# Kernel optimization log

Hardware: AMD Instinct MI355X
Metric: run time of the kernel (lower is better)

## Reference

```python
import jax, jax.numpy as jnp
import numpy as np

T, B, H, L = 64, 128, 256, 2  # steps/stack_size, batch, hidden, layers


def setup_inputs() -> dict:
    key = jax.random.key(0)
    ks = jax.random.split(key, 6)
    s = 1.0 / np.sqrt(H)
    x = jax.random.normal(ks[0], (T, B, H), dtype=jnp.float32)
    ops = jax.random.randint(ks[1], (T, B), 0, 2, dtype=jnp.int32)  # push=1, hold=0
    W_ih = jax.random.uniform(ks[2], (L, 4 * H, H), jnp.float32, -s, s)
    W_hh = jax.random.uniform(ks[3], (L, 4 * H, H), jnp.float32, -s, s)
    b_ih = jax.random.uniform(ks[4], (L, 4 * H), jnp.float32, -s, s)
    b_hh = jax.random.uniform(ks[5], (L, 4 * H), jnp.float32, -s, s)
    return {"x": x, "ops": ops, "W_ih": W_ih, "W_hh": W_hh, "b_ih": b_ih, "b_hh": b_hh}


def reference(x, ops, W_ih, W_hh, b_ih, b_hh):
    T_, B_, H_ = x.shape
    L_ = W_ih.shape[0]
    bidx = jnp.arange(B_)

    def cell(xt, h_prev, c_prev):
        # multi-layer LSTM cell; layer l>0 takes layer l-1 hidden as input (dropout=0)
        inp = xt
        hs, cs = [], []
        for l in range(L_):
            gates = inp @ W_ih[l].T + b_ih[l] + h_prev[..., l] @ W_hh[l].T + b_hh[l]
            i, f, g, o = jnp.split(gates, 4, axis=-1)
            c = jax.nn.sigmoid(f) * c_prev[..., l] + jax.nn.sigmoid(i) * jnp.tanh(g)
            h = jax.nn.sigmoid(o) * jnp.tanh(c)
            hs.append(h)
            cs.append(c)
            inp = h
        return jnp.stack(hs, axis=-1), jnp.stack(cs, axis=-1)  # (B, H, L)

    def step(carry, xt_op):
        hstack, cstack, pos = carry  # stacks: (T+1, B, H, L), pos: (B,)
        xt, opt = xt_op
        h_prev = hstack[pos, bidx]  # gather top-of-stack, (B, H, L)
        c_prev = cstack[pos, bidx]
        nh, nc = cell(xt, h_prev, c_prev)
        # hold_or_push writes at pos+1 for every batch element, then pos += op
        hstack = hstack.at[pos + 1, bidx].set(nh)
        cstack = cstack.at[pos + 1, bidx].set(nc)
        pos = pos + opt
        return (hstack, cstack, pos), nh[..., -1]  # last-layer hidden output

    hs0 = jnp.zeros((T_ + 1, B_, H_, L_), dtype=x.dtype)
    cs0 = jnp.zeros((T_ + 1, B_, H_, L_), dtype=x.dtype)
    pos0 = jnp.zeros((B_,), dtype=jnp.int32)
    _, outs = jax.lax.scan(step, (hs0, cs0, pos0), (x, ops))
    return outs  # (T, B, H)
```

## Files before the change

### kernel.cpp

```cpp
#include <hip/hip_runtime.h>
#include <hip/hip_fp16.h>
#include <cstddef>

#define TT 64
#define BB 128
#define HH 256
#define G4 1024
#define BLK 256
#define NBG 32
#define NHG 16

#define OFF_XG     0u
#define OFF_WTIH0  8388608u
#define OFF_HX0    8650752u
#define OFF_HX1    8716288u

__device__ __forceinline__ float sigf(float x) { return 1.0f / (1.0f + expf(-x)); }

typedef _Float16 h2v __attribute__((ext_vector_type(2)));

__device__ __forceinline__ float dot2acc(unsigned w, unsigned h, float acc) {
#if __has_builtin(__builtin_amdgcn_fdot2)
  return __builtin_amdgcn_fdot2(__builtin_bit_cast(h2v, w),
                                __builtin_bit_cast(h2v, h), acc, false);
#else
  __half2 wv = *(__half2*)&w, hv = *(__half2*)&h;
  float2 wf = __half22float2(wv), hf = __half22float2(hv);
  return fmaf(wf.x, hf.x, fmaf(wf.y, hf.y, acc));
#endif
}

__device__ __forceinline__ unsigned packh2(float e, float o) {
  return (unsigned)__half_as_ushort(__float2half(e)) |
         ((unsigned)__half_as_ushort(__float2half(o)) << 16);
}

__global__ void transpose1(const float* __restrict__ W_ih, float* __restrict__ ws) {
  __shared__ float tile[32][33];
  float* dst = ws + OFF_WTIH0;
  const int g0 = blockIdx.x * 32, k0 = blockIdx.y * 32;
  const int tx = threadIdx.x, ty = threadIdx.y;
#pragma unroll
  for (int i = 0; i < 32; i += 8)
    tile[ty + i][tx] = W_ih[(size_t)(g0 + ty + i) * HH + k0 + tx];
  __syncthreads();
#pragma unroll
  for (int i = 0; i < 32; i += 8)
    dst[(size_t)(k0 + ty + i) * G4 + g0 + tx] = tile[tx][ty + i];
}

__global__ void xg_kernel(const float* __restrict__ x,
                          const float* __restrict__ b_ih,
                          float* __restrict__ ws) {
  const float* __restrict__ WTih0 = ws + OFF_WTIH0;
  float* __restrict__ Xg = ws + OFF_XG;
  const int r0 = blockIdx.x * 16;
  const int g = blockIdx.y * 256 + threadIdx.x;
  __shared__ float xs[16][HH];
  for (int i = threadIdx.x; i < 16 * HH; i += 256)
    xs[i >> 8][i & 255] = x[(size_t)(r0 + (i >> 8)) * HH + (i & 255)];
  __syncthreads();
  float acc[16];
  const float bias = b_ih[g];
#pragma unroll
  for (int r = 0; r < 16; ++r) acc[r] = bias;
  for (int k = 0; k < HH; ++k) {
    const float w = WTih0[(size_t)k * G4 + g];
#pragma unroll
    for (int r = 0; r < 16; ++r) acc[r] = fmaf(xs[r][k], w, acc[r]);
  }
  const int hg = (g >> 4) & 15;
  const int lc = ((g >> 8) << 4) | (g & 15);
#pragma unroll
  for (int r = 0; r < 16; ++r) {
    const int rr = r0 + r;
    const int t = rr >> 7, b = rr & 127;
    Xg[(((size_t)t * NHG + hg) * 128 + b) * 64 + lc] = acc[r];
  }
}

__global__ void __launch_bounds__(BLK, 2)
seq7(const float* __restrict__ W_ih,
     const float* __restrict__ W_hh,
     const float* __restrict__ b_ih,
     const float* __restrict__ b_hh,
     const int* __restrict__ ops,
     float* __restrict__ ws,
     float* __restrict__ out) {
  const int bg = blockIdx.x & 31;
  const int hg = blockIdx.x >> 5;
  const int tid = threadIdx.x;
  const int kq = tid & 7;
  const int c2 = tid >> 3;

  __shared__ float XgL[TT * 256];
  __shared__ unsigned hp0[512];
  __shared__ unsigned hp1[512];
  __shared__ unsigned h0c[512];
  __shared__ float gat[256];
  __shared__ int opsA[TT * 4];

  unsigned wr0[32], wr1[32], wr2[32];
  {
    const float* s0 = W_hh;
    const float* s1 = W_ih + (size_t)G4 * HH;
    const float* s2 = W_hh + (size_t)G4 * HH;
#pragma unroll
    for (int j = 0; j < 2; ++j) {
      const int lc = c2 * 2 + j;
      const int g = ((lc >> 4) << 8) + hg * 16 + (lc & 15);
      const float* p0 = s0 + (size_t)g * HH + kq * 32;
      const float* p1 = s1 + (size_t)g * HH + kq * 32;
      const float* p2 = s2 + (size_t)g * HH + kq * 32;
#pragma unroll
      for (int i = 0; i < 16; ++i) {
        wr0[j * 16 + i] = packh2(p0[2 * i], p0[2 * i + 1]);
        wr1[j * 16 + i] = packh2(p1[2 * i], p1[2 * i + 1]);
        wr2[j * 16 + i] = packh2(p2[2 * i], p2[2 * i + 1]);
      }
    }
  }
  float bias0r[2], bias1r[2];
#pragma unroll
  for (int j = 0; j < 2; ++j) {
    const int lc = c2 * 2 + j;
    const int g = ((lc >> 4) << 8) + hg * 16 + (lc & 15);
    bias0r[j] = b_hh[g];
    bias1r[j] = b_ih[G4 + g] + b_hh[G4 + g];
  }
  for (int i = tid; i < TT * 64; i += BLK) {
    const int t = i >> 6, r = i & 63;
    ((float4*)XgL)[i] = *(const float4*)(
        ws + OFF_XG + (((size_t)t * NHG + hg) * 128 + bg * 4) * 64 + r * 4);
  }
  for (int i = tid; i < TT * 4; i += BLK)
    opsA[i] = ops[(i >> 2) * BB + bg * 4 + (i & 3)];
  for (int i = tid; i < 512; i += BLK) { hp0[i] = 0u; hp1[i] = 0u; }

  unsigned long long* __restrict__ Hx0 = (unsigned long long*)(ws + OFF_HX0);
  unsigned long long* __restrict__ Hx1 = (unsigned long long*)(ws + OFF_HX1);
  float cp0 = 0.f, cp1 = 0.f;
  __syncthreads();

  for (int t = 0; t < TT; ++t) {
    const int par = t & 1;

    float a0[4][2];
#pragma unroll
    for (int b = 0; b < 4; ++b) {
      const uint4 x0 = *(const uint4*)&hp0[b * 128 + kq * 16];
      const uint4 x1 = *(const uint4*)&hp0[b * 128 + kq * 16 + 4];
      const uint4 x2 = *(const uint4*)&hp0[b * 128 + kq * 16 + 8];
      const uint4 x3 = *(const uint4*)&hp0[b * 128 + kq * 16 + 12];
      const unsigned hh[16] = {x0.x, x0.y, x0.z, x0.w, x1.x, x1.y, x1.z, x1.w,
                               x2.x, x2.y, x2.z, x2.w, x3.x, x3.y, x3.z, x3.w};
#pragma unroll
      for (int j = 0; j < 2; ++j) {
        float a = 0.f;
#pragma unroll
        for (int i = 0; i < 16; ++i) a = dot2acc(wr0[j * 16 + i], hh[i], a);
        a0[b][j] = a;
      }
    }
#pragma unroll
    for (int m = 1; m <= 4; m <<= 1)
#pragma unroll
      for (int b = 0; b < 4; ++b) {
        a0[b][0] += __shfl_xor(a0[b][0], m, 64);
        a0[b][1] += __shfl_xor(a0[b][1], m, 64);
      }
    if (kq == 0) {
#pragma unroll
      for (int b = 0; b < 4; ++b)
        *(float2*)&gat[b * 64 + c2 * 2] =
            make_float2(a0[b][0] + bias0r[0], a0[b][1] + bias0r[1]);
    }
    __syncthreads();

    if (tid < 64) {
      const int b = tid >> 4, r = tid & 15;
      const float* xg = &XgL[t * 256 + b * 64];
      const float* gt = &gat[b * 64];
      const float ig = gt[r] + xg[r],           fg = gt[16 + r] + xg[16 + r];
      const float gg = gt[32 + r] + xg[32 + r], og = gt[48 + r] + xg[48 + r];
      const float c = sigf(fg) * cp0 + sigf(ig) * tanhf(gg);
      const float h = sigf(og) * tanhf(c);
      if (opsA[t * 4 + b]) cp0 = c;
      const float ho = __shfl_xor(h, 1, 64);
      if (!(r & 1)) {
        const unsigned long long v =
            (unsigned long long)(unsigned)(t + 1) |
            ((unsigned long long)packh2(h, ho) << 32);
        __hip_atomic_store(
            Hx0 + ((size_t)par * NBG + bg) * 512 + b * 128 + hg * 8 + (r >> 1),
            v, __ATOMIC_RELAXED, __HIP_MEMORY_SCOPE_AGENT);
      }
    }

    {
      const unsigned long long* s0 = Hx0 + ((size_t)par * NBG + bg) * 512;
      const unsigned tagA = (unsigned)(t + 1);
#pragma unroll
      for (int i = 0; i < 2; ++i) {
        const int idx = tid + i * 256;
        const int b = idx >> 7, k2 = idx & 127;
        unsigned long long v;
        int spins = 0;
        for (;;) {
          v = __hip_atomic_load(s0 + idx, __ATOMIC_RELAXED,
                                __HIP_MEMORY_SCOPE_AGENT);
          if ((unsigned)v == tagA) break;
          if (++spins > (1 << 18)) break;
          __builtin_amdgcn_s_sleep(1);
        }
        const unsigned pay = (unsigned)(v >> 32);
        h0c[b * 128 + k2] = pay;
        if (opsA[t * 4 + b]) hp0[b * 128 + k2] = pay;
      }
      if (t > 0) {
        const unsigned long long* s1 = Hx1 + ((size_t)(par ^ 1) * NBG + bg) * 512;
        const unsigned tagB = (unsigned)t;
#pragma unroll
        for (int i = 0; i < 2; ++i) {
          const int idx = tid + i * 256;
          const int b = idx >> 7, k2 = idx & 127;
          unsigned long long v;
          int spins = 0;
          for (;;) {
            v = __hip_atomic_load(s1 + idx, __ATOMIC_RELAXED,
                                  __HIP_MEMORY_SCOPE_AGENT);
            if ((unsigned)v == tagB) break;
            if (++spins > (1 << 18)) break;
            __builtin_amdgcn_s_sleep(1);
          }
          if (opsA[(t - 1) * 4 + b]) hp1[b * 128 + k2] = (unsigned)(v >> 32);
        }
      }
    }
    __syncthreads();

    float a1[4][2];
#pragma unroll
    for (int b = 0; b < 4; ++b) {
      const uint4 c0 = *(const uint4*)&h0c[b * 128 + kq * 16];
      const uint4 c1 = *(const uint4*)&h0c[b * 128 + kq * 16 + 4];
      const uint4 c2v = *(const uint4*)&h0c[b * 128 + kq * 16 + 8];
      const uint4 c3 = *(const uint4*)&h0c[b * 128 + kq * 16 + 12];
      const uint4 q0 = *(const uint4*)&hp1[b * 128 + kq * 16];
      const uint4 q1 = *(const uint4*)&hp1[b * 128 + kq * 16 + 4];
      const uint4 q2 = *(const uint4*)&hp1[b * 128 + kq * 16 + 8];
      const uint4 q3 = *(const uint4*)&hp1[b * 128 + kq * 16 + 12];
      const unsigned hc[16] = {c0.x, c0.y, c0.z, c0.w, c1.x, c1.y, c1.z, c1.w,
                               c2v.x, c2v.y, c2v.z, c2v.w, c3.x, c3.y, c3.z, c3.w};
      const unsigned hq[16] = {q0.x, q0.y, q0.z, q0.w, q1.x, q1.y, q1.z, q1.w,
                               q2.x, q2.y, q2.z, q2.w, q3.x, q3.y, q3.z, q3.w};
#pragma unroll
      for (int j = 0; j < 2; ++j) {
        float a = 0.f;
#pragma unroll
        for (int i = 0; i < 16; ++i) {
          a = dot2acc(wr1[j * 16 + i], hc[i], a);
          a = dot2acc(wr2[j * 16 + i], hq[i], a);
        }
        a1[b][j] = a;
      }
    }
#pragma unroll
    for (int m = 1; m <= 4; m <<= 1)
#pragma unroll
      for (int b = 0; b < 4; ++b) {
        a1[b][0] += __shfl_xor(a1[b][0], m, 64);
        a1[b][1] += __shfl_xor(a1[b][1], m, 64);
      }
    if (kq == 0) {
#pragma unroll
      for (int b = 0; b < 4; ++b)
        *(float2*)&gat[b * 64 + c2 * 2] =
            make_float2(a1[b][0] + bias1r[0], a1[b][1] + bias1r[1]);
    }
    __syncthreads();

    if (tid < 64) {
      const int b = tid >> 4, r = tid & 15;
      const float* gt = &gat[b * 64];
      const float ig = gt[r],      fg = gt[16 + r];
      const float gg = gt[32 + r], og = gt[48 + r];
      const float c = sigf(fg) * cp1 + sigf(ig) * tanhf(gg);
      const float h = sigf(og) * tanhf(c);
      if (opsA[t * 4 + b]) cp1 = c;
      out[((size_t)t * BB + bg * 4 + b) * HH + hg * 16 + r] = h;
      const float ho = __shfl_xor(h, 1, 64);
      if (!(r & 1)) {
        const unsigned long long v =
            (unsigned long long)(unsigned)(t + 1) |
            ((unsigned long long)packh2(h, ho) << 32);
        __hip_atomic_store(
            Hx1 + ((size_t)par * NBG + bg) * 512 + b * 128 + hg * 8 + (r >> 1),
            v, __ATOMIC_RELAXED, __HIP_MEMORY_SCOPE_AGENT);
      }
    }
    __syncthreads();
  }
}

extern "C" void kernel_launch(void* const* d_in, const int* in_sizes, int n_in,
                              void* d_out, int out_size, void* d_ws, size_t ws_size,
                              hipStream_t stream) {
  const float* x    = (const float*)d_in[0];
  const int*   ops  = (const int*)d_in[1];
  const float* W_ih = (const float*)d_in[2];
  const float* W_hh = (const float*)d_in[3];
  const float* b_ih = (const float*)d_in[4];
  const float* b_hh = (const float*)d_in[5];
  float* out = (float*)d_out;
  float* ws  = (float*)d_ws;

  transpose1<<<dim3(32, 8), dim3(32, 8), 0, stream>>>(W_ih, ws);
  xg_kernel<<<dim3(512, 4), 256, 0, stream>>>(x, b_ih, ws);
  seq7<<<512, BLK, 0, stream>>>(W_ih, W_hh, b_ih, b_hh, ops, ws, out);
}
```

Measured before the change: 554.7 us.

## Skip recurrent matvecs on hold steps, pad LDS rows, double-buffer gate scratch

```diff
diff --git a/kernel.cpp b/kernel.cpp
--- a/kernel.cpp
+++ b/kernel.cpp
@@ -35,6 +35,10 @@
          ((unsigned)__half_as_ushort(__float2half(o)) << 16);
 }
 
+__device__ __forceinline__ int hsw(int b, int k2) {
+  return b * 144 + k2 + ((k2 >> 5) << 2);
+}
+
 __global__ void transpose1(const float* __restrict__ W_ih, float* __restrict__ ws) {
   __shared__ float tile[32][33];
   float* dst = ws + OFF_WTIH0;
@@ -56,7 +60,7 @@
   float* __restrict__ Xg = ws + OFF_XG;
   const int r0 = blockIdx.x * 16;
   const int g = blockIdx.y * 256 + threadIdx.x;
-  __shared__ float xs[16][HH];
+  __shared__ __align__(16) float xs[16][HH];
   for (int i = threadIdx.x; i < 16 * HH; i += 256)
     xs[i >> 8][i & 255] = x[(size_t)(r0 + (i >> 8)) * HH + (i & 255)];
   __syncthreads();
@@ -64,10 +68,21 @@
   const float bias = b_ih[g];
 #pragma unroll
   for (int r = 0; r < 16; ++r) acc[r] = bias;
-  for (int k = 0; k < HH; ++k) {
-    const float w = WTih0[(size_t)k * G4 + g];
-#pragma unroll
-    for (int r = 0; r < 16; ++r) acc[r] = fmaf(xs[r][k], w, acc[r]);
+  for (int k = 0; k < HH; k += 4) {
+    const float w0 = WTih0[(size_t)k * G4 + g];
+    const float w1 = WTih0[(size_t)(k + 1) * G4 + g];
+    const float w2 = WTih0[(size_t)(k + 2) * G4 + g];
+    const float w3 = WTih0[(size_t)(k + 3) * G4 + g];
+#pragma unroll
+    for (int r = 0; r < 16; ++r) {
+      const float4 xv = *(const float4*)&xs[r][k];
+      float a = acc[r];
+      a = fmaf(xv.x, w0, a);
+      a = fmaf(xv.y, w1, a);
+      a = fmaf(xv.z, w2, a);
+      a = fmaf(xv.w, w3, a);
+      acc[r] = a;
+    }
   }
   const int hg = (g >> 4) & 15;
   const int lc = ((g >> 8) << 4) | (g & 15);
@@ -80,7 +95,7 @@
 }
 
 __global__ void __launch_bounds__(BLK, 2)
-seq7(const float* __restrict__ W_ih,
+seq8(const float* __restrict__ W_ih,
      const float* __restrict__ W_hh,
      const float* __restrict__ b_ih,
      const float* __restrict__ b_hh,
@@ -93,11 +108,12 @@
   const int kq = tid & 7;
   const int c2 = tid >> 3;
 
-  __shared__ float XgL[TT * 256];
-  __shared__ unsigned hp0[512];
-  __shared__ unsigned hp1[512];
-  __shared__ unsigned h0c[512];
-  __shared__ float gat[256];
+  __shared__ __align__(16) float XgL[TT * 256];
+  __shared__ __align__(16) unsigned hp0[4 * 144];
+  __shared__ __align__(16) unsigned hp1[4 * 144];
+  __shared__ __align__(16) unsigned h0c[4 * 144];
+  __shared__ float gatA[256];
+  __shared__ float gatB[256];
   __shared__ int opsA[TT * 4];
 
   unsigned wr0[32], wr1[32], wr2[32];
@@ -135,52 +151,55 @@
   }
   for (int i = tid; i < TT * 4; i += BLK)
     opsA[i] = ops[(i >> 2) * BB + bg * 4 + (i & 3)];
-  for (int i = tid; i < 512; i += BLK) { hp0[i] = 0u; hp1[i] = 0u; }
+  for (int i = tid; i < 4 * 144; i += BLK) { hp0[i] = 0u; hp1[i] = 0u; }
 
   unsigned long long* __restrict__ Hx0 = (unsigned long long*)(ws + OFF_HX0);
   unsigned long long* __restrict__ Hx1 = (unsigned long long*)(ws + OFF_HX1);
   float cp0 = 0.f, cp1 = 0.f;
+  float a0r[4][2] = {{0.f, 0.f}, {0.f, 0.f}, {0.f, 0.f}, {0.f, 0.f}};
+  float a1q[4][2] = {{0.f, 0.f}, {0.f, 0.f}, {0.f, 0.f}, {0.f, 0.f}};
   __syncthreads();
 
   for (int t = 0; t < TT; ++t) {
     const int par = t & 1;
 
-    float a0[4][2];
 #pragma unroll
     for (int b = 0; b < 4; ++b) {
-      const uint4 x0 = *(const uint4*)&hp0[b * 128 + kq * 16];
-      const uint4 x1 = *(const uint4*)&hp0[b * 128 + kq * 16 + 4];
-      const uint4 x2 = *(const uint4*)&hp0[b * 128 + kq * 16 + 8];
-      const uint4 x3 = *(const uint4*)&hp0[b * 128 + kq * 16 + 12];
-      const unsigned hh[16] = {x0.x, x0.y, x0.z, x0.w, x1.x, x1.y, x1.z, x1.w,
-                               x2.x, x2.y, x2.z, x2.w, x3.x, x3.y, x3.z, x3.w};
-#pragma unroll
-      for (int j = 0; j < 2; ++j) {
-        float a = 0.f;
-#pragma unroll
-        for (int i = 0; i < 16; ++i) a = dot2acc(wr0[j * 16 + i], hh[i], a);
-        a0[b][j] = a;
-      }
-    }
-#pragma unroll
-    for (int m = 1; m <= 4; m <<= 1)
-#pragma unroll
-      for (int b = 0; b < 4; ++b) {
-        a0[b][0] += __shfl_xor(a0[b][0], m, 64);
-        a0[b][1] += __shfl_xor(a0[b][1], m, 64);
-      }
+      if (t > 0 && opsA[(t - 1) * 4 + b]) {
+        const unsigned* hb = &hp0[b * 144 + kq * 16 + ((kq >> 1) << 2)];
+        const uint4 x0 = *(const uint4*)(hb + 0);
+        const uint4 x1 = *(const uint4*)(hb + 4);
+        const uint4 x2 = *(const uint4*)(hb + 8);
+        const uint4 x3 = *(const uint4*)(hb + 12);
+        const unsigned hh[16] = {x0.x, x0.y, x0.z, x0.w, x1.x, x1.y, x1.z, x1.w,
+                                 x2.x, x2.y, x2.z, x2.w, x3.x, x3.y, x3.z, x3.w};
+        float s0 = 0.f, s1 = 0.f;
+#pragma unroll
+        for (int i = 0; i < 16; ++i) {
+          s0 = dot2acc(wr0[i], hh[i], s0);
+          s1 = dot2acc(wr0[16 + i], hh[i], s1);
+        }
+#pragma unroll
+        for (int m = 1; m <= 4; m <<= 1) {
+          s0 += __shfl_xor(s0, m, 64);
+          s1 += __shfl_xor(s1, m, 64);
+        }
+        a0r[b][0] = s0;
+        a0r[b][1] = s1;
+      }
+    }
     if (kq == 0) {
 #pragma unroll
       for (int b = 0; b < 4; ++b)
-        *(float2*)&gat[b * 64 + c2 * 2] =
-            make_float2(a0[b][0] + bias0r[0], a0[b][1] + bias0r[1]);
+        *(float2*)&gatA[b * 64 + c2 * 2] =
+            make_float2(a0r[b][0] + bias0r[0], a0r[b][1] + bias0r[1]);
     }
     __syncthreads();
 
     if (tid < 64) {
       const int b = tid >> 4, r = tid & 15;
       const float* xg = &XgL[t * 256 + b * 64];
-      const float* gt = &gat[b * 64];
+      const float* gt = &gatA[b * 64];
       const float ig = gt[r] + xg[r],           fg = gt[16 + r] + xg[16 + r];
       const float gg = gt[32 + r] + xg[32 + r], og = gt[48 + r] + xg[48 + r];
       const float c = sigf(fg) * cp0 + sigf(ig) * tanhf(gg);
@@ -200,23 +219,34 @@
     {
       const unsigned long long* s0 = Hx0 + ((size_t)par * NBG + bg) * 512;
       const unsigned tagA = (unsigned)(t + 1);
-#pragma unroll
-      for (int i = 0; i < 2; ++i) {
-        const int idx = tid + i * 256;
-        const int b = idx >> 7, k2 = idx & 127;
-        unsigned long long v;
-        int spins = 0;
-        for (;;) {
-          v = __hip_atomic_load(s0 + idx, __ATOMIC_RELAXED,
-                                __HIP_MEMORY_SCOPE_AGENT);
-          if ((unsigned)v == tagA) break;
-          if (++spins > (1 << 18)) break;
-          __builtin_amdgcn_s_sleep(1);
-        }
-        const unsigned pay = (unsigned)(v >> 32);
-        h0c[b * 128 + k2] = pay;
-        if (opsA[t * 4 + b]) hp0[b * 128 + k2] = pay;
-      }
+      const int idx1 = tid + 256;
+      const int b0 = tid >> 7, k20 = tid & 127;
+      const int b1 = idx1 >> 7, k21 = idx1 & 127;
+      unsigned long long v0 = __hip_atomic_load(s0 + tid, __ATOMIC_RELAXED,
+                                                __HIP_MEMORY_SCOPE_AGENT);
+      unsigned long long v1 = __hip_atomic_load(s0 + idx1, __ATOMIC_RELAXED,
+                                                __HIP_MEMORY_SCOPE_AGENT);
+      int spins = 0;
+      while ((unsigned)v0 != tagA) {
+        if (++spins > (1 << 18)) break;
+        __builtin_amdgcn_s_sleep(1);
+        v0 = __hip_atomic_load(s0 + tid, __ATOMIC_RELAXED,
+                               __HIP_MEMORY_SCOPE_AGENT);
+      }
+      spins = 0;
+      while ((unsigned)v1 != tagA) {
+        if (++spins > (1 << 18)) break;
+        __builtin_amdgcn_s_sleep(1);
+        v1 = __hip_atomic_load(s0 + idx1, __ATOMIC_RELAXED,
+                               __HIP_MEMORY_SCOPE_AGENT);
+      }
+      const unsigned p0 = (unsigned)(v0 >> 32), p1 = (unsigned)(v1 >> 32);
+      const int sw0 = hsw(b0, k20), sw1 = hsw(b1, k21);
+      h0c[sw0] = p0;
+      h0c[sw1] = p1;
+      if (opsA[t * 4 + b0]) hp0[sw0] = p0;
+      if (opsA[t * 4 + b1]) hp0[sw1] = p1;
+
       if (t > 0) {
         const unsigned long long* s1 = Hx1 + ((size_t)(par ^ 1) * NBG + bg) * 512;
         const unsigned tagB = (unsigned)t;
@@ -224,73 +254,90 @@
         for (int i = 0; i < 2; ++i) {
           const int idx = tid + i * 256;
           const int b = idx >> 7, k2 = idx & 127;
-          unsigned long long v;
-          int spins = 0;
-          for (;;) {
-            v = __hip_atomic_load(s1 + idx, __ATOMIC_RELAXED,
-                                  __HIP_MEMORY_SCOPE_AGENT);
-            if ((unsigned)v == tagB) break;
-            if (++spins > (1 << 18)) break;
-            __builtin_amdgcn_s_sleep(1);
+          if (opsA[(t - 1) * 4 + b]) {
+            unsigned long long v;
+            int sp = 0;
+            for (;;) {
+              v = __hip_atomic_load(s1 + idx, __ATOMIC_RELAXED,
+                                    __HIP_MEMORY_SCOPE_AGENT);
+              if ((unsigned)v == tagB) break;
+              if (++sp > (1 << 18)) break;
+              __builtin_amdgcn_s_sleep(1);
+            }
+            hp1[hsw(b, k2)] = (unsigned)(v >> 32);
           }
-          if (opsA[(t - 1) * 4 + b]) hp1[b * 128 + k2] = (unsigned)(v >> 32);
         }
       }
     }
     __syncthreads();
 
-    float a1[4][2];
+    float fr[4][2];
 #pragma unroll
     for (int b = 0; b < 4; ++b) {
-      const uint4 c0 = *(const uint4*)&h0c[b * 128 + kq * 16];
-      const uint4 c1 = *(const uint4*)&h0c[b * 128 + kq * 16 + 4];
-      const uint4 c2v = *(const uint4*)&h0c[b * 128 + kq * 16 + 8];
-      const uint4 c3 = *(const uint4*)&h0c[b * 128 + kq * 16 + 12];
-      const uint4 q0 = *(const uint4*)&hp1[b * 128 + kq * 16];
-      const uint4 q1 = *(const uint4*)&hp1[b * 128 + kq * 16 + 4];
-      const uint4 q2 = *(const uint4*)&hp1[b * 128 + kq * 16 + 8];
-      const uint4 q3 = *(const uint4*)&hp1[b * 128 + kq * 16 + 12];
+      const unsigned* cb = &h0c[b * 144 + kq * 16 + ((kq >> 1) << 2)];
+      const uint4 c0 = *(const uint4*)(cb + 0);
+      const uint4 c1 = *(const uint4*)(cb + 4);
+      const uint4 c2v = *(const uint4*)(cb + 8);
+      const uint4 c3 = *(const uint4*)(cb + 12);
       const unsigned hc[16] = {c0.x, c0.y, c0.z, c0.w, c1.x, c1.y, c1.z, c1.w,
                                c2v.x, c2v.y, c2v.z, c2v.w, c3.x, c3.y, c3.z, c3.w};
-      const unsigned hq[16] = {q0.x, q0.y, q0.z, q0.w, q1.x, q1.y, q1.z, q1.w,
-                               q2.x, q2.y, q2.z, q2.w, q3.x, q3.y, q3.z, q3.w};
-#pragma unroll
-      for (int j = 0; j < 2; ++j) {
-        float a = 0.f;
+      float s0 = 0.f, s1 = 0.f;
+#pragma unroll
+      for (int i = 0; i < 16; ++i) {
+        s0 = dot2acc(wr1[i], hc[i], s0);
+        s1 = dot2acc(wr1[16 + i], hc[i], s1);
+      }
+      if (t > 0 && opsA[(t - 1) * 4 + b]) {
+        const unsigned* qb = &hp1[b * 144 + kq * 16 + ((kq >> 1) << 2)];
+        const uint4 q0 = *(const uint4*)(qb + 0);
+        const uint4 q1 = *(const uint4*)(qb + 4);
+        const uint4 q2 = *(const uint4*)(qb + 8);
+        const uint4 q3 = *(const uint4*)(qb + 12);
+        const unsigned hq[16] = {q0.x, q0.y, q0.z, q0.w, q1.x, q1.y, q1.z, q1.w,
+                                 q2.x, q2.y, q2.z, q2.w, q3.x, q3.y, q3.z, q3.w};
+        float t0 = 0.f, t1 = 0.f;
 #pragma unroll
         for (int i = 0; i < 16; ++i) {
-          a = dot2acc(wr1[j * 16 + i], hc[i], a);
-          a = dot2acc(wr2[j * 16 + i], hq[i], a);
-        }
-        a1[b][j] = a;
-      }
-    }
-#pragma unroll
-    for (int m = 1; m <= 4; m <<= 1)
-#pragma unroll
-      for (int b = 0; b < 4; ++b) {
-        a1[b][0] += __shfl_xor(a1[b][0], m, 64);
-        a1[b][1] += __shfl_xor(a1[b][1], m, 64);
-      }
+          t0 = dot2acc(wr2[i], hq[i], t0);
+          t1 = dot2acc(wr2[16 + i], hq[i], t1);
+        }
+#pragma unroll
+        for (int m = 1; m <= 4; m <<= 1) {
+          t0 += __shfl_xor(t0, m, 64);
+          t1 += __shfl_xor(t1, m, 64);
+        }
+        a1q[b][0] = t0;
+        a1q[b][1] = t1;
+      }
+#pragma unroll
+      for (int m = 1; m <= 4; m <<= 1) {
+        s0 += __shfl_xor(s0, m, 64);
+        s1 += __shfl_xor(s1, m, 64);
+      }
+      fr[b][0] = s0;
+      fr[b][1] = s1;
+    }
     if (kq == 0) {
 #pragma unroll
       for (int b = 0; b < 4; ++b)
-        *(float2*)&gat[b * 64 + c2 * 2] =
-            make_float2(a1[b][0] + bias1r[0], a1[b][1] + bias1r[1]);
+        *(float2*)&gatB[b * 64 + c2 * 2] =
+            make_float2(fr[b][0] + a1q[b][0] + bias1r[0],
+                        fr[b][1] + a1q[b][1] + bias1r[1]);
     }
     __syncthreads();
 
     if (tid < 64) {
       const int b = tid >> 4, r = tid & 15;
-      const float* gt = &gat[b * 64];
+      const float* gt = &gatB[b * 64];
       const float ig = gt[r],      fg = gt[16 + r];
       const float gg = gt[32 + r], og = gt[48 + r];
       const float c = sigf(fg) * cp1 + sigf(ig) * tanhf(gg);
       const float h = sigf(og) * tanhf(c);
-      if (opsA[t * 4 + b]) cp1 = c;
+      const int op = opsA[t * 4 + b];
+      if (op) cp1 = c;
       out[((size_t)t * BB + bg * 4 + b) * HH + hg * 16 + r] = h;
       const float ho = __shfl_xor(h, 1, 64);
-      if (!(r & 1)) {
+      if (op && !(r & 1)) {
         const unsigned long long v =
             (unsigned long long)(unsigned)(t + 1) |
             ((unsigned long long)packh2(h, ho) << 32);
@@ -299,7 +346,6 @@
             v, __ATOMIC_RELAXED, __HIP_MEMORY_SCOPE_AGENT);
       }
     }
-    __syncthreads();
   }
 }
 
@@ -317,5 +363,5 @@
 
   transpose1<<<dim3(32, 8), dim3(32, 8), 0, stream>>>(W_ih, ws);
   xg_kernel<<<dim3(512, 4), 256, 0, stream>>>(x, b_ih, ws);
-  seq7<<<512, BLK, 0, stream>>>(W_ih, W_hh, b_ih, b_hh, ops, ws, out);
-}
+  seq8<<<512, BLK, 0, stream>>>(W_ih, W_hh, b_ih, b_hh, ops, ws, out);
+}
```

Result: slower. 571.0 us (+2.9%).
